# Kernel optimization log

Measured on AMD Instinct MI355X. Metric: run time of the kernel, lower is better.

## Reference

```python
import jax, jax.numpy as jnp
import numpy as np

B, NQ, NKV = 8, 256, 1024
DQ, DK, DV = 256, 256, 256
H = 128  # num_hiddens
NEG_INF = -1e20


def setup_inputs() -> dict:
    key = jax.random.key(0)
    k1, k2, k3, k4, k5, k6, k7 = jax.random.split(key, 7)
    s = 0.05
    return {
        "Q_batch": jax.random.normal(k1, (B, NQ, DQ), jnp.float32),
        "K_batch": jax.random.normal(k2, (B, NKV, DK), jnp.float32),
        "V_batch": jax.random.normal(k3, (B, NKV, DV), jnp.float32),
        "valid_lens": jax.random.randint(k4, (B,), 1, NKV, jnp.int32),
        # Learned params (torch nn.Linear stores weight as (out, in); no bias)
        "Wq": jax.random.normal(k5, (H, DQ), jnp.float32) * s,
        "Wk": jax.random.normal(k6, (H, DK), jnp.float32) * s,
        "Wv": jax.random.normal(k7, (H,), jnp.float32) * s,  # W_v: Linear(H -> 1)
    }


def reference(Q_batch, K_batch, V_batch, valid_lens, Wq, Wk, Wv):
    # Project queries and keys to hidden size H
    q = jnp.einsum('bqd,hd->bqh', Q_batch, Wq)            # (B, NQ, H)
    k = jnp.einsum('bkd,hd->bkh', K_batch, Wk)            # (B, NKV, H)
    # Broadcast add -> tanh -> score projection (materializes (B,NQ,NKV,H))
    S = jnp.tanh(q[:, :, None, :] + k[:, None, :, :])     # (B, NQ, NKV, H)
    scores = jnp.einsum('bqkh,h->bqk', S, Wv)             # (B, NQ, NKV)
    # Masked softmax: 'left' => positions >= valid_len are invalid
    kv_idx = jnp.arange(NKV)                              # (NKV,)
    mask = kv_idx[None, None, :] >= valid_lens[:, None, None]  # (B,1,NKV) broadcast over queries
    scores = jnp.where(mask, NEG_INF, scores)
    attn = jax.nn.softmax(scores, axis=-1)                # (B, NQ, NKV)
    # Dropout is identity in eval mode (rate 0.0)
    return jnp.einsum('bqk,bkv->bqv', attn, V_batch)      # (B, NQ, DV)
```

## Files before the change

kernel.cpp:

```cpp
#include <hip/hip_runtime.h>
#include <hip/hip_bf16.h>
#include <math.h>

#define BB   8
#define NQ   256
#define NKV  1024
#define DD   256
#define HH   128
#define KSPLIT 4
#define KCH  256

typedef float f16v __attribute__((ext_vector_type(16)));

__global__ __launch_bounds__(256) void proj_exp_kernel(
    const float* __restrict__ Q, const float* __restrict__ K,
    const float* __restrict__ Wq, const float* __restrict__ Wk,
    float* __restrict__ eqb, float* __restrict__ ekb)
{
    __shared__ __align__(16) float At[32][20];
    __shared__ __align__(16) float Wt[32][132];

    const int bid = blockIdx.x;
    const bool isQ = bid < (BB * NQ / 16);
    const float* A = isQ ? Q : K;
    const float* W = isQ ? Wq : Wk;
    float* Out     = isQ ? eqb : ekb;
    const int arow0 = (isQ ? bid : bid - (BB * NQ / 16)) * 16;

    const int tid = threadIdx.x;
    const int rc  = tid >> 5;
    const int hc  = tid & 31;

    float4 c0 = {0.f,0.f,0.f,0.f}, c1 = c0;

    float4 a4;
    float4 w4[4];

    if (tid < 128)
        a4 = *(const float4*)(A + (size_t)(arow0 + (tid >> 3)) * DD + (tid & 7) * 4);
#pragma unroll
    for (int t = 0; t < 4; ++t) {
        int idx = tid + t * 256;
        int h = idx >> 3, dw = idx & 7;
        w4[t] = *(const float4*)(W + (size_t)h * DD + dw * 4);
    }

    for (int ch = 0; ch < 8; ++ch) {
        __syncthreads();
        if (tid < 128) {
            int r_st = tid >> 3, dq = tid & 7;
            At[dq*4+0][r_st] = a4.x;
            At[dq*4+1][r_st] = a4.y;
            At[dq*4+2][r_st] = a4.z;
            At[dq*4+3][r_st] = a4.w;
        }
#pragma unroll
        for (int t = 0; t < 4; ++t) {
            int idx = tid + t * 256;
            int h = idx >> 3, dw = idx & 7;
            Wt[dw*4+0][h] = w4[t].x;
            Wt[dw*4+1][h] = w4[t].y;
            Wt[dw*4+2][h] = w4[t].z;
            Wt[dw*4+3][h] = w4[t].w;
        }
        __syncthreads();
        if (ch + 1 < 8) {
            const int dc = (ch + 1) * 32;
            if (tid < 128)
                a4 = *(const float4*)(A + (size_t)(arow0 + (tid >> 3)) * DD + dc + (tid & 7) * 4);
#pragma unroll
            for (int t = 0; t < 4; ++t) {
                int idx = tid + t * 256;
                int h = idx >> 3, dw = idx & 7;
                w4[t] = *(const float4*)(W + (size_t)h * DD + dc + dw * 4);
            }
        }
#pragma unroll
        for (int d = 0; d < 32; ++d) {
            float a0  = At[d][rc];
            float a1  = At[d][rc + 8];
            float4 wv = *(const float4*)&Wt[d][hc * 4];
            c0.x = fmaf(a0, wv.x, c0.x); c0.y = fmaf(a0, wv.y, c0.y);
            c0.z = fmaf(a0, wv.z, c0.z); c0.w = fmaf(a0, wv.w, c0.w);
            c1.x = fmaf(a1, wv.x, c1.x); c1.y = fmaf(a1, wv.y, c1.y);
            c1.z = fmaf(a1, wv.z, c1.z); c1.w = fmaf(a1, wv.w, c1.w);
        }
    }

    float4 o;
    float* p0 = Out + (size_t)(arow0 + rc) * HH + hc * 4;
    o.x = __expf(2.f*c0.x); o.y = __expf(2.f*c0.y);
    o.z = __expf(2.f*c0.z); o.w = __expf(2.f*c0.w);
    *(float4*)p0 = o;
    float* p1 = Out + (size_t)(arow0 + rc + 8) * HH + hc * 4;
    o.x = __expf(2.f*c1.x); o.y = __expf(2.f*c1.y);
    o.z = __expf(2.f*c1.z); o.w = __expf(2.f*c1.w);
    *(float4*)p1 = o;
}

__global__ __launch_bounds__(512) void attn_partial_kernel(
    const float* __restrict__ V, const int* __restrict__ vls,
    const float* __restrict__ Wv,
    const float* __restrict__ eqb, const float* __restrict__ ekb,
    float* __restrict__ pvb, float* __restrict__ mlb)
{
    __shared__ __align__(16) float sc[8][KCH];
    __shared__ __align__(16) float red[4][8][KCH];

    const int bid  = blockIdx.x;
    const int s    = bid & (KSPLIT - 1);
    const int t    = bid >> 2;
    const int b    = t >> 5;
    const int k0   = s << 8;
    const int r0   = t * 8;
    const int tid  = threadIdx.x;
    const int w    = tid >> 6;
    const int lane = tid & 63;
    const int vl   = vls[b];

    if (k0 >= vl) {
        float4 z = {0.f, 0.f, 0.f, 0.f};
        ((float4*)(pvb + ((size_t)(r0 + w) * KSPLIT + s) * KCH))[lane] = z;
        if (lane == 0) {
            mlb[((r0 + w) * KSPLIT + s) * 2 + 0] = -1e30f;
            mlb[((r0 + w) * KSPLIT + s) * 2 + 1] = 0.f;
        }
        return;
    }

    const int qg = w & 1;
    const int ks = ((w >> 1) << 3) + (lane >> 3);
    const int hg = lane & 7;

    const int kcnt = min(vl - k0, KCH);
    const int nst  = (kcnt + 31) >> 5;

    f16v nw2;
    float swv = 0.f;
#pragma unroll
    for (int i = 0; i < 4; ++i) {
        float4 v4 = *(const float4*)(Wv + hg * 16 + i * 4);
        nw2[i*4+0] = -2.f * v4.x; nw2[i*4+1] = -2.f * v4.y;
        nw2[i*4+2] = -2.f * v4.z; nw2[i*4+3] = -2.f * v4.w;
        swv += v4.x + v4.y + v4.z + v4.w;
    }

    f16v eqr[4];
#pragma unroll
    for (int r = 0; r < 4; ++r) {
        const float4* p = (const float4*)(eqb + (size_t)(r0 + qg*4 + r) * HH + hg * 16);
        float4 x0 = p[0], x1 = p[1], x2 = p[2], x3 = p[3];
        f16v e;
        e[0]=x0.x;e[1]=x0.y;e[2]=x0.z;e[3]=x0.w; e[4]=x1.x;e[5]=x1.y;e[6]=x1.z;e[7]=x1.w;
        e[8]=x2.x;e[9]=x2.y;e[10]=x2.z;e[11]=x2.w; e[12]=x3.x;e[13]=x3.y;e[14]=x3.z;e[15]=x3.w;
        eqr[r] = e;
    }

    const float* ekbase = ekb + ((size_t)(b * NKV) + k0) * HH + hg * 16;

    auto loadEk = [&](f16v& e, int step) {
        const float4* p = (const float4*)(ekbase + (size_t)(step * 32 + ks) * HH);
        float4 x0 = p[0], x1 = p[1], x2 = p[2], x3 = p[3];
        e[0]=x0.x;e[1]=x0.y;e[2]=x0.z;e[3]=x0.w; e[4]=x1.x;e[5]=x1.y;e[6]=x1.z;e[7]=x1.w;
        e[8]=x2.x;e[9]=x2.y;e[10]=x2.z;e[11]=x2.w; e[12]=x3.x;e[13]=x3.y;e[14]=x3.z;e[15]=x3.w;
    };

    auto body = [&](const f16v& e, int step) {
        float a0 = swv, a1 = swv, a2 = swv, a3 = swv;
#pragma unroll
        for (int j = 0; j < 16; ++j) {
            float ej = e[j];
            float t0 = fmaf(eqr[0][j], ej, 1.0f);
            float t1 = fmaf(eqr[1][j], ej, 1.0f);
            float t2 = fmaf(eqr[2][j], ej, 1.0f);
            float t3 = fmaf(eqr[3][j], ej, 1.0f);
            float r0v = __builtin_amdgcn_rcpf(t0);
            float r1v = __builtin_amdgcn_rcpf(t1);
            float r2v = __builtin_amdgcn_rcpf(t2);
            float r3v = __builtin_amdgcn_rcpf(t3);
            float nj = nw2[j];
            a0 = fmaf(nj, r0v, a0);
            a1 = fmaf(nj, r1v, a1);
            a2 = fmaf(nj, r2v, a2);
            a3 = fmaf(nj, r3v, a3);
        }
        a0 += __shfl_xor(a0, 1); a0 += __shfl_xor(a0, 2); a0 += __shfl_xor(a0, 4);
        a1 += __shfl_xor(a1, 1); a1 += __shfl_xor(a1, 2); a1 += __shfl_xor(a1, 4);
        a2 += __shfl_xor(a2, 1); a2 += __shfl_xor(a2, 2); a2 += __shfl_xor(a2, 4);
        a3 += __shfl_xor(a3, 1); a3 += __shfl_xor(a3, 2); a3 += __shfl_xor(a3, 4);
        if (hg == 0) {
            int kk = step * 32 + ks;
            sc[qg*4+0][kk] = a0;
            sc[qg*4+1][kk] = a1;
            sc[qg*4+2][kk] = a2;
            sc[qg*4+3][kk] = a3;
        }
    };

    f16v ekA, ekB;
    loadEk(ekA, 0);
    for (int st = 0; st < nst; st += 2) {
        if (st + 1 < nst) loadEk(ekB, st + 1);
        body(ekA, st);
        if (st + 1 < nst) {
            if (st + 2 < nst) loadEk(ekA, st + 2);
            body(ekB, st + 1);
        }
    }
    __syncthreads();

    {
        float m = -1e30f;
        float sv[4];
#pragma unroll
        for (int i = 0; i < 4; ++i) {
            int kk = i * 64 + lane;
            float sval = sc[w][kk];
            sv[i] = sval;
            if (k0 + kk < vl) m = fmaxf(m, sval);
        }
#pragma unroll
        for (int off = 1; off < 64; off <<= 1) m = fmaxf(m, __shfl_xor(m, off));
        float sum = 0.f;
#pragma unroll
        for (int i = 0; i < 4; ++i) {
            int kk = i * 64 + lane;
            float p = (k0 + kk < vl) ? __expf(sv[i] - m) : 0.f;
            sum += p;
            sc[w][kk] = p;
        }
#pragma unroll
        for (int off = 1; off < 64; off <<= 1) sum += __shfl_xor(sum, off);
        if (lane == 0) {
            mlb[((r0 + w) * KSPLIT + s) * 2 + 0] = m;
            mlb[((r0 + w) * KSPLIT + s) * 2 + 1] = sum;
        }
    }
    __syncthreads();

    float4 acc[8];
#pragma unroll
    for (int r = 0; r < 8; ++r) acc[r] = make_float4(0.f, 0.f, 0.f, 0.f);
    {
        const int kbase = w * 32;
        if (kbase < kcnt) {
            const float* vb = V + ((size_t)b * NKV + k0 + kbase) * DD + lane * 4;
            for (int kk = 0; kk < 32; kk += 4) {
                float4 pr[8];
#pragma unroll
                for (int r = 0; r < 8; ++r)
                    pr[r] = *(const float4*)&sc[r][kbase + kk];
#pragma unroll
                for (int u = 0; u < 4; ++u) {
                    float4 vv = *(const float4*)(vb + (size_t)(kk + u) * DD);
#pragma unroll
                    for (int r = 0; r < 8; ++r) {
                        float p = (u == 0) ? pr[r].x : (u == 1) ? pr[r].y
                                : (u == 2) ? pr[r].z : pr[r].w;
                        acc[r].x = fmaf(p, vv.x, acc[r].x);
                        acc[r].y = fmaf(p, vv.y, acc[r].y);
                        acc[r].z = fmaf(p, vv.z, acc[r].z);
                        acc[r].w = fmaf(p, vv.w, acc[r].w);
                    }
                }
            }
        }
    }
    if (w < 4) {
#pragma unroll
        for (int r = 0; r < 8; ++r)
            *(float4*)&red[w][r][lane * 4] = acc[r];
    }
    __syncthreads();
    if (w >= 4) {
#pragma unroll
        for (int r = 0; r < 8; ++r) {
            float4 tv = *(const float4*)&red[w - 4][r][lane * 4];
            tv.x += acc[r].x; tv.y += acc[r].y;
            tv.z += acc[r].z; tv.w += acc[r].w;
            *(float4*)&red[w - 4][r][lane * 4] = tv;
        }
    }
    __syncthreads();
    {
        float4 o = {0.f, 0.f, 0.f, 0.f};
#pragma unroll
        for (int ss = 0; ss < 4; ++ss) {
            float4 tv = *(const float4*)&red[ss][w][lane * 4];
            o.x += tv.x; o.y += tv.y; o.z += tv.z; o.w += tv.w;
        }
        ((float4*)(pvb + ((size_t)(r0 + w) * KSPLIT + s) * KCH))[lane] = o;
    }
}

__global__ __launch_bounds__(256) void combine_kernel(
    const float* __restrict__ pvb, const float* __restrict__ mlb,
    float* __restrict__ out)
{
    const int tid  = threadIdx.x;
    const int r    = blockIdx.x * 4 + (tid >> 6);
    const int lane = tid & 63;

    float mv[KSPLIT], lv[KSPLIT];
#pragma unroll
    for (int s = 0; s < KSPLIT; ++s) {
        mv[s] = mlb[(r * KSPLIT + s) * 2 + 0];
        lv[s] = mlb[(r * KSPLIT + s) * 2 + 1];
    }
    float M = fmaxf(fmaxf(mv[0], mv[1]), fmaxf(mv[2], mv[3]));
    float coef[KSPLIT];
    float L = 0.f;
#pragma unroll
    for (int s = 0; s < KSPLIT; ++s) {
        coef[s] = __expf(mv[s] - M);
        L = fmaf(lv[s], coef[s], L);
    }
    float rinv = 1.0f / L;

    float4 acc = {0.f, 0.f, 0.f, 0.f};
#pragma unroll
    for (int s = 0; s < KSPLIT; ++s) {
        float4 pv = ((const float4*)(pvb + ((size_t)r * KSPLIT + s) * KCH))[lane];
        float cs = coef[s];
        acc.x = fmaf(cs, pv.x, acc.x);
        acc.y = fmaf(cs, pv.y, acc.y);
        acc.z = fmaf(cs, pv.z, acc.z);
        acc.w = fmaf(cs, pv.w, acc.w);
    }
    acc.x *= rinv; acc.y *= rinv; acc.z *= rinv; acc.w *= rinv;
    *(float4*)(out + (size_t)r * DD + lane * 4) = acc;
}

extern "C" void kernel_launch(void* const* d_in, const int* in_sizes, int n_in,
                              void* d_out, int out_size, void* d_ws, size_t ws_size,
                              hipStream_t stream) {
    const float* Q   = (const float*)d_in[0];
    const float* K   = (const float*)d_in[1];
    const float* V   = (const float*)d_in[2];
    const int*   vls = (const int*)  d_in[3];
    const float* Wq  = (const float*)d_in[4];
    const float* Wk  = (const float*)d_in[5];
    const float* Wv  = (const float*)d_in[6];
    float* out = (float*)d_out;

    float* eq = (float*)d_ws;
    float* ek = eq + (size_t)BB * NQ * HH;
    float* pv = ek + (size_t)BB * NKV * HH;
    float* ml = pv + (size_t)BB * NQ * KSPLIT * KCH;

    proj_exp_kernel<<<(BB*NQ + BB*NKV) / 16, 256, 0, stream>>>(Q, K, Wq, Wk, eq, ek);
    attn_partial_kernel<<<BB * (NQ / 8) * KSPLIT, 512, 0, stream>>>(V, vls, Wv, eq, ek, pv, ml);
    combine_kernel<<<BB * NQ / 4, 256, 0, stream>>>(pv, ml, out);
}
```

Baseline: 163.6 us.

## Make attention partial kernel persistent with atomic work queue

The attention partial kernel now launches a fixed grid of persistent blocks. Each block pulls work items off a global atomic counter, with the item order changed so the split index is the outermost dimension. Blocks whose key chunk lies entirely past the valid length now only write the max/sum sentinels, not zeroed partial outputs. The goal is to balance the uneven per-item work caused by the varying valid lengths, at the cost of a memset, an atomic per item and extra block syncs.

```diff
diff --git a/kernel.cpp b/kernel.cpp
--- a/kernel.cpp
+++ b/kernel.cpp
@@ -9,6 +9,8 @@
 #define HH   128
 #define KSPLIT 4
 #define KCH  256
+#define NITEMS (BB * (NQ / 8) * KSPLIT)
+#define NWORK  512
 
 typedef float f16v __attribute__((ext_vector_type(16)));
 
@@ -102,38 +104,19 @@
     const float* __restrict__ V, const int* __restrict__ vls,
     const float* __restrict__ Wv,
     const float* __restrict__ eqb, const float* __restrict__ ekb,
-    float* __restrict__ pvb, float* __restrict__ mlb)
+    float* __restrict__ pvb, float* __restrict__ mlb,
+    unsigned int* __restrict__ qcnt)
 {
     __shared__ __align__(16) float sc[8][KCH];
     __shared__ __align__(16) float red[4][8][KCH];
-
-    const int bid  = blockIdx.x;
-    const int s    = bid & (KSPLIT - 1);
-    const int t    = bid >> 2;
-    const int b    = t >> 5;
-    const int k0   = s << 8;
-    const int r0   = t * 8;
+    __shared__ int curs;
+
     const int tid  = threadIdx.x;
     const int w    = tid >> 6;
     const int lane = tid & 63;
-    const int vl   = vls[b];
-
-    if (k0 >= vl) {
-        float4 z = {0.f, 0.f, 0.f, 0.f};
-        ((float4*)(pvb + ((size_t)(r0 + w) * KSPLIT + s) * KCH))[lane] = z;
-        if (lane == 0) {
-            mlb[((r0 + w) * KSPLIT + s) * 2 + 0] = -1e30f;
-            mlb[((r0 + w) * KSPLIT + s) * 2 + 1] = 0.f;
-        }
-        return;
-    }
-
     const int qg = w & 1;
     const int ks = ((w >> 1) << 3) + (lane >> 3);
     const int hg = lane & 7;
-
-    const int kcnt = min(vl - k0, KCH);
-    const int nst  = (kcnt + 31) >> 5;
 
     f16v nw2;
     float swv = 0.f;
@@ -145,151 +128,177 @@
         swv += v4.x + v4.y + v4.z + v4.w;
     }
 
-    f16v eqr[4];
-#pragma unroll
-    for (int r = 0; r < 4; ++r) {
-        const float4* p = (const float4*)(eqb + (size_t)(r0 + qg*4 + r) * HH + hg * 16);
-        float4 x0 = p[0], x1 = p[1], x2 = p[2], x3 = p[3];
-        f16v e;
-        e[0]=x0.x;e[1]=x0.y;e[2]=x0.z;e[3]=x0.w; e[4]=x1.x;e[5]=x1.y;e[6]=x1.z;e[7]=x1.w;
-        e[8]=x2.x;e[9]=x2.y;e[10]=x2.z;e[11]=x2.w; e[12]=x3.x;e[13]=x3.y;e[14]=x3.z;e[15]=x3.w;
-        eqr[r] = e;
-    }
-
-    const float* ekbase = ekb + ((size_t)(b * NKV) + k0) * HH + hg * 16;
-
-    auto loadEk = [&](f16v& e, int step) {
-        const float4* p = (const float4*)(ekbase + (size_t)(step * 32 + ks) * HH);
-        float4 x0 = p[0], x1 = p[1], x2 = p[2], x3 = p[3];
-        e[0]=x0.x;e[1]=x0.y;e[2]=x0.z;e[3]=x0.w; e[4]=x1.x;e[5]=x1.y;e[6]=x1.z;e[7]=x1.w;
-        e[8]=x2.x;e[9]=x2.y;e[10]=x2.z;e[11]=x2.w; e[12]=x3.x;e[13]=x3.y;e[14]=x3.z;e[15]=x3.w;
-    };
-
-    auto body = [&](const f16v& e, int step) {
-        float a0 = swv, a1 = swv, a2 = swv, a3 = swv;
-#pragma unroll
-        for (int j = 0; j < 16; ++j) {
-            float ej = e[j];
-            float t0 = fmaf(eqr[0][j], ej, 1.0f);
-            float t1 = fmaf(eqr[1][j], ej, 1.0f);
-            float t2 = fmaf(eqr[2][j], ej, 1.0f);
-            float t3 = fmaf(eqr[3][j], ej, 1.0f);
-            float r0v = __builtin_amdgcn_rcpf(t0);
-            float r1v = __builtin_amdgcn_rcpf(t1);
-            float r2v = __builtin_amdgcn_rcpf(t2);
-            float r3v = __builtin_amdgcn_rcpf(t3);
-            float nj = nw2[j];
-            a0 = fmaf(nj, r0v, a0);
-            a1 = fmaf(nj, r1v, a1);
-            a2 = fmaf(nj, r2v, a2);
-            a3 = fmaf(nj, r3v, a3);
-        }
-        a0 += __shfl_xor(a0, 1); a0 += __shfl_xor(a0, 2); a0 += __shfl_xor(a0, 4);
-        a1 += __shfl_xor(a1, 1); a1 += __shfl_xor(a1, 2); a1 += __shfl_xor(a1, 4);
-        a2 += __shfl_xor(a2, 1); a2 += __shfl_xor(a2, 2); a2 += __shfl_xor(a2, 4);
-        a3 += __shfl_xor(a3, 1); a3 += __shfl_xor(a3, 2); a3 += __shfl_xor(a3, 4);
-        if (hg == 0) {
-            int kk = step * 32 + ks;
-            sc[qg*4+0][kk] = a0;
-            sc[qg*4+1][kk] = a1;
-            sc[qg*4+2][kk] = a2;
-            sc[qg*4+3][kk] = a3;
-        }
-    };
-
-    f16v ekA, ekB;
-    loadEk(ekA, 0);
-    for (int st = 0; st < nst; st += 2) {
-        if (st + 1 < nst) loadEk(ekB, st + 1);
-        body(ekA, st);
-        if (st + 1 < nst) {
-            if (st + 2 < nst) loadEk(ekA, st + 2);
-            body(ekB, st + 1);
-        }
-    }
-    __syncthreads();
-
-    {
-        float m = -1e30f;
-        float sv[4];
-#pragma unroll
-        for (int i = 0; i < 4; ++i) {
-            int kk = i * 64 + lane;
-            float sval = sc[w][kk];
-            sv[i] = sval;
-            if (k0 + kk < vl) m = fmaxf(m, sval);
-        }
-#pragma unroll
-        for (int off = 1; off < 64; off <<= 1) m = fmaxf(m, __shfl_xor(m, off));
-        float sum = 0.f;
-#pragma unroll
-        for (int i = 0; i < 4; ++i) {
-            int kk = i * 64 + lane;
-            float p = (k0 + kk < vl) ? __expf(sv[i] - m) : 0.f;
-            sum += p;
-            sc[w][kk] = p;
-        }
-#pragma unroll
-        for (int off = 1; off < 64; off <<= 1) sum += __shfl_xor(sum, off);
-        if (lane == 0) {
-            mlb[((r0 + w) * KSPLIT + s) * 2 + 0] = m;
-            mlb[((r0 + w) * KSPLIT + s) * 2 + 1] = sum;
-        }
-    }
-    __syncthreads();
-
-    float4 acc[8];
-#pragma unroll
-    for (int r = 0; r < 8; ++r) acc[r] = make_float4(0.f, 0.f, 0.f, 0.f);
-    {
-        const int kbase = w * 32;
-        if (kbase < kcnt) {
-            const float* vb = V + ((size_t)b * NKV + k0 + kbase) * DD + lane * 4;
-            for (int kk = 0; kk < 32; kk += 4) {
-                float4 pr[8];
-#pragma unroll
-                for (int r = 0; r < 8; ++r)
-                    pr[r] = *(const float4*)&sc[r][kbase + kk];
-#pragma unroll
-                for (int u = 0; u < 4; ++u) {
-                    float4 vv = *(const float4*)(vb + (size_t)(kk + u) * DD);
-#pragma unroll
-                    for (int r = 0; r < 8; ++r) {
-                        float p = (u == 0) ? pr[r].x : (u == 1) ? pr[r].y
-                                : (u == 2) ? pr[r].z : pr[r].w;
-                        acc[r].x = fmaf(p, vv.x, acc[r].x);
-                        acc[r].y = fmaf(p, vv.y, acc[r].y);
-                        acc[r].z = fmaf(p, vv.z, acc[r].z);
-                        acc[r].w = fmaf(p, vv.w, acc[r].w);
+    for (;;) {
+        __syncthreads();
+        if (tid == 0) curs = (int)atomicAdd(qcnt, 1u);
+        __syncthreads();
+        const int idx = curs;
+        if (idx >= NITEMS) break;
+
+        const int s  = idx >> 8;
+        const int t  = idx & 255;
+        const int b  = t >> 5;
+        const int k0 = s << 8;
+        const int r0 = t * 8;
+        const int vl = vls[b];
+
+        if (k0 >= vl) {
+            if (tid < 8) {
+                mlb[((r0 + tid) * KSPLIT + s) * 2 + 0] = -1e30f;
+                mlb[((r0 + tid) * KSPLIT + s) * 2 + 1] = 0.f;
+            }
+            continue;
+        }
+
+        const int kcnt = min(vl - k0, KCH);
+        const int nst  = (kcnt + 31) >> 5;
+
+        f16v eqr[4];
+#pragma unroll
+        for (int r = 0; r < 4; ++r) {
+            const float4* p = (const float4*)(eqb + (size_t)(r0 + qg*4 + r) * HH + hg * 16);
+            float4 x0 = p[0], x1 = p[1], x2 = p[2], x3 = p[3];
+            f16v e;
+            e[0]=x0.x;e[1]=x0.y;e[2]=x0.z;e[3]=x0.w; e[4]=x1.x;e[5]=x1.y;e[6]=x1.z;e[7]=x1.w;
+            e[8]=x2.x;e[9]=x2.y;e[10]=x2.z;e[11]=x2.w; e[12]=x3.x;e[13]=x3.y;e[14]=x3.z;e[15]=x3.w;
+            eqr[r] = e;
+        }
+
+        const float* ekbase = ekb + ((size_t)(b * NKV) + k0) * HH + hg * 16;
+
+        auto loadEk = [&](f16v& e, int step) {
+            const float4* p = (const float4*)(ekbase + (size_t)(step * 32 + ks) * HH);
+            float4 x0 = p[0], x1 = p[1], x2 = p[2], x3 = p[3];
+            e[0]=x0.x;e[1]=x0.y;e[2]=x0.z;e[3]=x0.w; e[4]=x1.x;e[5]=x1.y;e[6]=x1.z;e[7]=x1.w;
+            e[8]=x2.x;e[9]=x2.y;e[10]=x2.z;e[11]=x2.w; e[12]=x3.x;e[13]=x3.y;e[14]=x3.z;e[15]=x3.w;
+        };
+
+        auto body = [&](const f16v& e, int step) {
+            float a0 = swv, a1 = swv, a2 = swv, a3 = swv;
+#pragma unroll
+            for (int j = 0; j < 16; ++j) {
+                float ej = e[j];
+                float t0 = fmaf(eqr[0][j], ej, 1.0f);
+                float t1 = fmaf(eqr[1][j], ej, 1.0f);
+                float t2 = fmaf(eqr[2][j], ej, 1.0f);
+                float t3 = fmaf(eqr[3][j], ej, 1.0f);
+                float r0v = __builtin_amdgcn_rcpf(t0);
+                float r1v = __builtin_amdgcn_rcpf(t1);
+                float r2v = __builtin_amdgcn_rcpf(t2);
+                float r3v = __builtin_amdgcn_rcpf(t3);
+                float nj = nw2[j];
+                a0 = fmaf(nj, r0v, a0);
+                a1 = fmaf(nj, r1v, a1);
+                a2 = fmaf(nj, r2v, a2);
+                a3 = fmaf(nj, r3v, a3);
+            }
+            a0 += __shfl_xor(a0, 1); a0 += __shfl_xor(a0, 2); a0 += __shfl_xor(a0, 4);
+            a1 += __shfl_xor(a1, 1); a1 += __shfl_xor(a1, 2); a1 += __shfl_xor(a1, 4);
+            a2 += __shfl_xor(a2, 1); a2 += __shfl_xor(a2, 2); a2 += __shfl_xor(a2, 4);
+            a3 += __shfl_xor(a3, 1); a3 += __shfl_xor(a3, 2); a3 += __shfl_xor(a3, 4);
+            if (hg == 0) {
+                int kk = step * 32 + ks;
+                sc[qg*4+0][kk] = a0;
+                sc[qg*4+1][kk] = a1;
+                sc[qg*4+2][kk] = a2;
+                sc[qg*4+3][kk] = a3;
+            }
+        };
+
+        f16v ekA, ekB;
+        loadEk(ekA, 0);
+        for (int st = 0; st < nst; st += 2) {
+            if (st + 1 < nst) loadEk(ekB, st + 1);
+            body(ekA, st);
+            if (st + 1 < nst) {
+                if (st + 2 < nst) loadEk(ekA, st + 2);
+                body(ekB, st + 1);
+            }
+        }
+        __syncthreads();
+
+        {
+            float m = -1e30f;
+            float sv[4];
+#pragma unroll
+            for (int i = 0; i < 4; ++i) {
+                int kk = i * 64 + lane;
+                float sval = sc[w][kk];
+                sv[i] = sval;
+                if (k0 + kk < vl) m = fmaxf(m, sval);
+            }
+#pragma unroll
+            for (int off = 1; off < 64; off <<= 1) m = fmaxf(m, __shfl_xor(m, off));
+            float sum = 0.f;
+#pragma unroll
+            for (int i = 0; i < 4; ++i) {
+                int kk = i * 64 + lane;
+                float p = (k0 + kk < vl) ? __expf(sv[i] - m) : 0.f;
+                sum += p;
+                sc[w][kk] = p;
+            }
+#pragma unroll
+            for (int off = 1; off < 64; off <<= 1) sum += __shfl_xor(sum, off);
+            if (lane == 0) {
+                mlb[((r0 + w) * KSPLIT + s) * 2 + 0] = m;
+                mlb[((r0 + w) * KSPLIT + s) * 2 + 1] = sum;
+            }
+        }
+        __syncthreads();
+
+        float4 acc[8];
+#pragma unroll
+        for (int r = 0; r < 8; ++r) acc[r] = make_float4(0.f, 0.f, 0.f, 0.f);
+        {
+            const int kbase = w * 32;
+            if (kbase < kcnt) {
+                const float* vb = V + ((size_t)b * NKV + k0 + kbase) * DD + lane * 4;
+                for (int kk = 0; kk < 32; kk += 4) {
+                    float4 pr[8];
+#pragma unroll
+                    for (int r = 0; r < 8; ++r)
+                        pr[r] = *(const float4*)&sc[r][kbase + kk];
+#pragma unroll
+                    for (int u = 0; u < 4; ++u) {
+                        float4 vv = *(const float4*)(vb + (size_t)(kk + u) * DD);
+#pragma unroll
+                        for (int r = 0; r < 8; ++r) {
+                            float p = (u == 0) ? pr[r].x : (u == 1) ? pr[r].y
+                                    : (u == 2) ? pr[r].z : pr[r].w;
+                            acc[r].x = fmaf(p, vv.x, acc[r].x);
+                            acc[r].y = fmaf(p, vv.y, acc[r].y);
+                            acc[r].z = fmaf(p, vv.z, acc[r].z);
+                            acc[r].w = fmaf(p, vv.w, acc[r].w);
+                        }
                     }
                 }
             }
         }
-    }
-    if (w < 4) {
-#pragma unroll
-        for (int r = 0; r < 8; ++r)
-            *(float4*)&red[w][r][lane * 4] = acc[r];
-    }
-    __syncthreads();
-    if (w >= 4) {
-#pragma unroll
-        for (int r = 0; r < 8; ++r) {
-            float4 tv = *(const float4*)&red[w - 4][r][lane * 4];
-            tv.x += acc[r].x; tv.y += acc[r].y;
-            tv.z += acc[r].z; tv.w += acc[r].w;
-            *(float4*)&red[w - 4][r][lane * 4] = tv;
-        }
-    }
-    __syncthreads();
-    {
-        float4 o = {0.f, 0.f, 0.f, 0.f};
-#pragma unroll
-        for (int ss = 0; ss < 4; ++ss) {
-            float4 tv = *(const float4*)&red[ss][w][lane * 4];
-            o.x += tv.x; o.y += tv.y; o.z += tv.z; o.w += tv.w;
-        }
-        ((float4*)(pvb + ((size_t)(r0 + w) * KSPLIT + s) * KCH))[lane] = o;
+        if (w < 4) {
+#pragma unroll
+            for (int r = 0; r < 8; ++r)
+                *(float4*)&red[w][r][lane * 4] = acc[r];
+        }
+        __syncthreads();
+        if (w >= 4) {
+#pragma unroll
+            for (int r = 0; r < 8; ++r) {
+                float4 tv = *(const float4*)&red[w - 4][r][lane * 4];
+                tv.x += acc[r].x; tv.y += acc[r].y;
+                tv.z += acc[r].z; tv.w += acc[r].w;
+                *(float4*)&red[w - 4][r][lane * 4] = tv;
+            }
+        }
+        __syncthreads();
+        {
+            float4 o = {0.f, 0.f, 0.f, 0.f};
+#pragma unroll
+            for (int ss = 0; ss < 4; ++ss) {
+                float4 tv = *(const float4*)&red[ss][w][lane * 4];
+                o.x += tv.x; o.y += tv.y; o.z += tv.z; o.w += tv.w;
+            }
+            ((float4*)(pvb + ((size_t)(r0 + w) * KSPLIT + s) * KCH))[lane] = o;
+        }
     }
 }
 
@@ -347,8 +356,10 @@
     float* ek = eq + (size_t)BB * NQ * HH;
     float* pv = ek + (size_t)BB * NKV * HH;
     float* ml = pv + (size_t)BB * NQ * KSPLIT * KCH;
-
+    unsigned int* qcnt = (unsigned int*)(ml + (size_t)BB * NQ * KSPLIT * 2);
+
+    hipMemsetAsync(qcnt, 0, sizeof(unsigned int), stream);
     proj_exp_kernel<<<(BB*NQ + BB*NKV) / 16, 256, 0, stream>>>(Q, K, Wq, Wk, eq, ek);
-    attn_partial_kernel<<<BB * (NQ / 8) * KSPLIT, 512, 0, stream>>>(V, vls, Wv, eq, ek, pv, ml);
+    attn_partial_kernel<<<NWORK, 512, 0, stream>>>(V, vls, Wv, eq, ek, pv, ml, qcnt);
     combine_kernel<<<BB * NQ / 4, 256, 0, stream>>>(pv, ml, out);
 }
```

New measurement: 144.5 us. 1.13x faster.
